# Kernel optimization log

Hardware: AMD Instinct MI355X
Metric: run time of the kernel (lower is better)

The kernel has to match this reference:

```python
import jax, jax.numpy as jnp
import numpy as np

Q = 3
MAX_SHIFT = 4.0


def setup_inputs() -> dict:
    key = jax.random.key(0)
    k1, k2, k3, k4 = jax.random.split(key, 4)
    x = jax.random.normal(k1, (16, 64, 128, 128), jnp.float32)
    weight = jax.random.normal(k2, (64, 192, 3, 3), jnp.float32) * 0.05
    bias = jax.random.normal(k3, (64,), jnp.float32) * 0.05
    # shift_init='random': uniform in [-1, 1]; forward multiplies by max_shift
    shifts = jax.random.uniform(k4, (64, 2), jnp.float32, -1.0, 1.0)
    return {"x": x, "weight": weight, "bias": bias, "shifts": shifts}


def _shift_bilinear(x, shifts, max_shift):
    """Per-channel bilinear translation, matching affine_grid+grid_sample
    (align_corners=False, padding_mode='zeros').
    x: [N,C,H,W]; shifts: [C,2] with (sx, sy) in normalized units.
    Sample location for output (i,j) is (i + sy*max_shift, j + sx*max_shift)."""
    N, C, H, W = x.shape
    sx = shifts[:, 0] * max_shift  # pixels along width
    sy = shifts[:, 1] * max_shift  # pixels along height
    ys = jnp.arange(H, dtype=x.dtype)[None, :] + sy[:, None]  # [C,H]
    xs = jnp.arange(W, dtype=x.dtype)[None, :] + sx[:, None]  # [C,W]
    y0f = jnp.floor(ys); fy = ys - y0f; y0 = y0f.astype(jnp.int32); y1 = y0 + 1
    x0f = jnp.floor(xs); fx = xs - x0f; x0 = x0f.astype(jnp.int32); x1 = x0 + 1

    def gather(yi, xi):
        vy = (yi >= 0) & (yi < H)          # [C,H]
        vx = (xi >= 0) & (xi < W)          # [C,W]
        yc = jnp.clip(yi, 0, H - 1)
        xc = jnp.clip(xi, 0, W - 1)
        g = jnp.take_along_axis(x, yc[None, :, :, None], axis=2)
        g = jnp.take_along_axis(g, xc[None, :, None, :], axis=3)
        m = (vy[:, :, None] & vx[:, None, :]).astype(x.dtype)[None]
        return g * m

    w00 = ((1 - fy)[:, :, None] * (1 - fx)[:, None, :])[None]
    w01 = ((1 - fy)[:, :, None] * fx[:, None, :])[None]
    w10 = (fy[:, :, None] * (1 - fx)[:, None, :])[None]
    w11 = (fy[:, :, None] * fx[:, None, :])[None]
    return (w00 * gather(y0, x0) + w01 * gather(y0, x1)
            + w10 * gather(y1, x0) + w11 * gather(y1, x1))


def reference(x, weight, bias, shifts):
    # 1) per-channel learnless shift (grid_sample bilinear, zeros padding)
    xs = _shift_bilinear(x, shifts, MAX_SHIFT)
    # 2) Maclaurin power series: concat(x, x^2, ..., x^q) on channels -> [N, C*q, H, W]
    xq = jnp.concatenate([xs ** i for i in range(1, Q + 1)], axis=1)
    # 3) dense conv (groups=1), stride 1, padding 1
    out = jax.lax.conv_general_dilated(
        xq, weight, window_strides=(1, 1), padding=((1, 1), (1, 1)),
        dimension_numbers=("NCHW", "OIHW", "NCHW"))
    return out + bias[None, :, None, None]
```

## Files before the change

kernel.cpp:

```cpp
#include <hip/hip_runtime.h>
#include <hip/hip_bf16.h>
#include <math.h>

#define NB 16
#define C_IN 64
#define C_OUT 64
#define HH 128
#define WW 128
#define MAX_SHIFT 4.0f

typedef __attribute__((ext_vector_type(8))) short bf16x8;
typedef __attribute__((ext_vector_type(4))) float f32x4;
typedef __attribute__((ext_vector_type(4))) unsigned int u32x4;

__device__ inline unsigned short bf16_rne(float f) {
    unsigned u = __builtin_bit_cast(unsigned, f);
    u += 0x7fffu + ((u >> 16) & 1u);
    return (unsigned short)(u >> 16);
}
__device__ inline unsigned pack_bf16x2(float lo, float hi) {
    unsigned ul = __builtin_bit_cast(unsigned, lo);
    unsigned uh = __builtin_bit_cast(unsigned, hi);
    ul += 0x7fffu + ((ul >> 16) & 1u);
    uh += 0x7fffu + ((uh >> 16) & 1u);
    return (ul >> 16) | (uh & 0xffff0000u);
}

#define VSTR 34

__global__ __launch_bounds__(256)
void shift_pow3(const float* __restrict__ x, const float* __restrict__ shifts,
                unsigned short* __restrict__ xsp) {
    __shared__ unsigned short row[128 * VSTR];
    __shared__ float s_fx[C_IN], s_fy[C_IN];
    __shared__ int s_dx[C_IN], s_dy[C_IN];

    int bid0 = blockIdx.x;
    int bid = (bid0 & 7) * 512 + (bid0 >> 3);
    int h  = bid & 127;
    int n  = (bid >> 7) & 15;
    int cg = bid >> 11;
    int tid = threadIdx.x;
    int wv = tid >> 6;
    int l  = tid & 63;

    if (tid < C_IN) {
        float sx = shifts[2 * tid] * MAX_SHIFT;
        float sy = shifts[2 * tid + 1] * MAX_SHIFT;
        float fx0 = floorf(sx), fy0 = floorf(sy);
        s_dx[tid] = (int)fx0; s_dy[tid] = (int)fy0;
        s_fx[tid] = sx - fx0;  s_fy[tid] = sy - fy0;
    }
    __syncthreads();

    const float* xn = x + (size_t)n * (C_IN * HH * WW);

    #pragma unroll 4
    for (int it = 0; it < 8; ++it) {
        int c32 = it * 4 + wv;
        int c   = cg * 32 + c32;
        int dx = s_dx[c], dy = s_dy[c];
        float fx = s_fx[c], fy = s_fy[c];
        const float* xp = xn + (size_t)c * (HH * WW);
        int y0 = h + dy, y1 = y0 + 1;
        bool vy0 = ((unsigned)y0 < (unsigned)HH);
        bool vy1 = ((unsigned)y1 < (unsigned)HH);
        const float* r0 = xp + y0 * WW;
        const float* r1 = xp + y1 * WW;

        #pragma unroll
        for (int hf = 0; hf < 2; ++hf) {
            int w = hf * 64 + l;
            int x0 = w + dx, x1 = x0 + 1;
            bool vx0 = ((unsigned)x0 < (unsigned)WW);
            bool vx1 = ((unsigned)x1 < (unsigned)WW);
            float v00 = (vy0 && vx0) ? r0[x0] : 0.f;
            float v01 = (vy0 && vx1) ? r0[x1] : 0.f;
            float v10 = (vy1 && vx0) ? r1[x0] : 0.f;
            float v11 = (vy1 && vx1) ? r1[x1] : 0.f;
            float v = (1.f - fy) * ((1.f - fx) * v00 + fx * v01)
                    + fy * ((1.f - fx) * v10 + fx * v11);
            row[w * VSTR + c32] = bf16_rne(v);
        }
    }
    __syncthreads();

    const unsigned* rp = (const unsigned*)row;
    unsigned* xsp32 = (unsigned*)xsp;
    #pragma unroll 1
    for (int p = 0; p < 3; ++p) {
        int kb = p * 2 + cg;
        unsigned* dst = xsp32 + (size_t)(kb * (NB * HH) + n * HH + h) * 2048;
        #pragma unroll
        for (int itw = 0; itw < 8; ++itw) {
            int o32 = itw * 256 + tid;
            int wl = o32 >> 4;
            int c4 = o32 & 15;
            unsigned u = rp[wl * 17 + c4];
            if (p != 0) {
                float f0 = __builtin_bit_cast(float, u << 16);
                float f1 = __builtin_bit_cast(float, u & 0xffff0000u);
                float r0 = f0 * f0, r1 = f1 * f1;
                if (p == 2) { r0 *= f0; r1 *= f1; }
                u = pack_bf16x2(r0, r1);
            }
            dst[o32] = u;
        }
    }
}

__global__ void prep_w2(const float* __restrict__ w, unsigned short* __restrict__ wbuf) {
    int id = blockIdx.x * 256 + threadIdx.x;
    int e = id & 7;
    int l = (id >> 3) & 63;
    int f = id >> 9;
    int mf = f & 3;
    int f2 = f >> 2;
    int kb = f2 % 6;
    int t  = f2 / 6;
    int k  = kb * 32 + (l >> 4) * 8 + e;
    int p  = k >> 6;
    int c  = k & 63;
    int co = mf * 16 + (l & 15);
    wbuf[id] = bf16_rne(w[(co * 192 + p * 64 + c) * 9 + t]);
}

__global__ __launch_bounds__(256, 2)
void conv2(const unsigned short* __restrict__ xsp,
           const unsigned short* __restrict__ wbuf,
           const float* __restrict__ bias,
           float* __restrict__ out) {
    __shared__ unsigned short tile[324 * 44];

    int bid = blockIdx.x;
    int wg = (bid & 7) * 128 + (bid >> 3);
    int n  = wg >> 6;
    int t6 = wg & 63;
    int i0 = (t6 >> 3) * 16;
    int j0 = (t6 & 7) * 16;

    int tid = threadIdx.x;
    int l  = tid & 63;
    int wv = tid >> 6;
    int lm = l & 15;
    int lg = l >> 4;

    f32x4 acc[4][4];
    #pragma unroll
    for (int mf = 0; mf < 4; ++mf) {
        #pragma unroll
        for (int r = 0; r < 4; ++r) {
            float bv = bias[mf * 16 + lg * 4 + r];
            #pragma unroll
            for (int nf = 0; nf < 4; ++nf) acc[mf][nf][r] = bv;
        }
    }

    int lds_base = (wv * 4 * 18 + lm) * 88 + lg * 16;

    #pragma unroll 1
    for (int kb = 0; kb < 6; ++kb) {
        const unsigned short* xr = xsp + (size_t)(kb * NB + n) * (HH * WW * 32);
        __syncthreads();
        #pragma unroll
        for (int it = 0; it < 6; ++it) {
            int ch = it * 256 + tid;
            if (ch < 1296) {
                int rr  = ch / 72;
                int rem = ch - rr * 72;
                int pxr = rem >> 2, sub = rem & 3;
                int gi = i0 - 1 + rr, gj = j0 - 1 + pxr;
                u32x4 d = {0, 0, 0, 0};
                if ((unsigned)gi < (unsigned)HH && (unsigned)gj < (unsigned)WW)
                    d = *(const u32x4*)(xr + ((size_t)gi * WW + gj) * 32 + sub * 8);
                *(u32x4*)((char*)tile + (rr * 18 + pxr) * 88 + sub * 16) = d;
            }
        }
        __syncthreads();

        __builtin_amdgcn_s_setprio(1);
        bf16x8 Af[4];
        #pragma unroll
        for (int mf = 0; mf < 4; ++mf)
            Af[mf] = *(const bf16x8*)(wbuf + (size_t)((0 * 6 + kb) * 4 + mf) * 512 + l * 8);

        #pragma unroll 1
        for (int t = 0; t < 9; ++t) {
            bf16x8 Afn[4];
            int tn = (t < 8) ? t + 1 : t;
            #pragma unroll
            for (int mf = 0; mf < 4; ++mf)
                Afn[mf] = *(const bf16x8*)(wbuf + (size_t)((tn * 6 + kb) * 4 + mf) * 512 + l * 8);

            int ky = t / 3, kx = t - ky * 3;
            #pragma unroll
            for (int nf = 0; nf < 4; ++nf) {
                int off = lds_base + ((nf + ky) * 18 + kx) * 88;
                bf16x8 bfrag = *(const bf16x8*)((const char*)tile + off);
                #pragma unroll
                for (int mf = 0; mf < 4; ++mf)
                    acc[mf][nf] = __builtin_amdgcn_mfma_f32_16x16x32_bf16(Af[mf], bfrag, acc[mf][nf], 0, 0, 0);
            }
            #pragma unroll
            for (int mf = 0; mf < 4; ++mf) Af[mf] = Afn[mf];
        }
        __builtin_amdgcn_s_setprio(0);
    }

    #pragma unroll
    for (int mf = 0; mf < 4; ++mf) {
        #pragma unroll
        for (int nf = 0; nf < 4; ++nf) {
            int rowi = i0 + wv * 4 + nf;
            int col = j0 + lm;
            #pragma unroll
            for (int r = 0; r < 4; ++r) {
                int co = mf * 16 + lg * 4 + r;
                out[(((size_t)n * C_OUT + co) * HH + rowi) * WW + col] = acc[mf][nf][r];
            }
        }
    }
}

#define S_PX 100

__global__ void prep_w3(const float* __restrict__ w, unsigned short* __restrict__ wbuf) {
    int id = blockIdx.x * 256 + threadIdx.x;
    int e = id & 7;
    int l = (id >> 3) & 63;
    int f = id >> 9;
    int mf = f & 3;
    int f2 = f >> 2;
    int kb = f2 % 6;
    int t  = f2 / 6;
    int cg = kb / 3;
    int p  = kb - cg * 3;
    int cl = (l >> 4) * 8 + e;
    int co = mf * 16 + (l & 15);
    wbuf[id] = bf16_rne(w[(co * 192 + p * 64 + cg * 32 + cl) * 9 + t]);
}

__global__ __launch_bounds__(256, 2)
void conv_f(const float* __restrict__ x,
            const float* __restrict__ shifts,
            const unsigned short* __restrict__ wbuf,
            const float* __restrict__ bias,
            float* __restrict__ out) {
    __shared__ unsigned short tile[324 * S_PX];
    __shared__ float s_fx[C_IN], s_fy[C_IN];
    __shared__ int s_dx[C_IN], s_dy[C_IN];

    int bid = blockIdx.x;
    int wg = (bid & 7) * 128 + (bid >> 3);
    int n  = wg >> 6;
    int t6 = wg & 63;
    int i0 = (t6 >> 3) * 16;
    int j0 = (t6 & 7) * 16;

    int tid = threadIdx.x;
    int l  = tid & 63;
    int wv = tid >> 6;
    int lm = l & 15;
    int lg = l >> 4;

    if (tid < C_IN) {
        float sx = shifts[2 * tid] * MAX_SHIFT;
        float sy = shifts[2 * tid + 1] * MAX_SHIFT;
        float fx0 = floorf(sx), fy0 = floorf(sy);
        s_dx[tid] = (int)fx0; s_dy[tid] = (int)fy0;
        s_fx[tid] = sx - fx0;  s_fy[tid] = sy - fy0;
    }

    f32x4 acc[4][4];
    #pragma unroll
    for (int mf = 0; mf < 4; ++mf) {
        #pragma unroll
        for (int r = 0; r < 4; ++r) {
            float bv = bias[mf * 16 + lg * 4 + r];
            #pragma unroll
            for (int nf = 0; nf < 4; ++nf) acc[mf][nf][r] = bv;
        }
    }

    const float* xn = x + (size_t)n * (C_IN * HH * WW);

    #pragma unroll 1
    for (int cg = 0; cg < 2; ++cg) {
        __syncthreads();
        #pragma unroll 2
        for (int it = 0; it < 21; ++it) {
            int item = it * 256 + tid;
            if (item < 5184) {
                int cl  = item / 162;
                int rem = item - cl * 162;
                int rp  = rem / 18;
                int cc  = rem - rp * 18;
                int c   = cg * 32 + cl;
                int dx = s_dx[c], dy = s_dy[c];
                float fx = s_fx[c], fy = s_fy[c];
                const float* xp = xn + (size_t)c * (HH * WW);

                int gj  = j0 - 1 + cc;
                int xx0 = gj + dx, xx1 = xx0 + 1;
                bool vx0 = ((unsigned)xx0 < (unsigned)WW);
                bool vx1 = ((unsigned)xx1 < (unsigned)WW);
                int gi0 = i0 - 1 + rp * 2;
                int y0  = gi0 + dy;
                bool vyA = ((unsigned)y0 < (unsigned)HH);
                bool vyB = ((unsigned)(y0 + 1) < (unsigned)HH);
                bool vyC = ((unsigned)(y0 + 2) < (unsigned)HH);
                const float* rA = xp + y0 * WW;
                const float* rB = rA + WW;
                const float* rC = rB + WW;
                float m0 = (vyA && vx0) ? rA[xx0] : 0.f;
                float m1 = (vyA && vx1) ? rA[xx1] : 0.f;
                float m2 = (vyB && vx0) ? rB[xx0] : 0.f;
                float m3 = (vyB && vx1) ? rB[xx1] : 0.f;
                float m4 = (vyC && vx0) ? rC[xx0] : 0.f;
                float m5 = (vyC && vx1) ? rC[xx1] : 0.f;
                float hA = (1.f - fx) * m0 + fx * m1;
                float hB = (1.f - fx) * m2 + fx * m3;
                float hC = (1.f - fx) * m4 + fx * m5;
                float vT = (1.f - fy) * hA + fy * hB;
                float vU = (1.f - fy) * hB + fy * hC;
                if (!((unsigned)gj < (unsigned)WW))        { vT = 0.f; vU = 0.f; }
                if (!((unsigned)gi0 < (unsigned)HH))       vT = 0.f;
                if (!((unsigned)(gi0 + 1) < (unsigned)HH)) vU = 0.f;

                float t2 = vT * vT, t3 = t2 * vT;
                float u2 = vU * vU, u3 = u2 * vU;
                unsigned short* recT = tile + (rp * 2 * 18 + cc) * S_PX;
                unsigned short* recU = recT + 18 * S_PX;
                recT[cl]      = bf16_rne(vT);
                recT[32 + cl] = bf16_rne(t2);
                recT[64 + cl] = bf16_rne(t3);
                recU[cl]      = bf16_rne(vU);
                recU[32 + cl] = bf16_rne(u2);
                recU[64 + cl] = bf16_rne(u3);
            }
        }
        __syncthreads();

        #pragma unroll 1
        for (int p = 0; p < 3; ++p) {
            int kb = cg * 3 + p;
            #pragma unroll 1
            for (int t = 0; t < 9; ++t) {
                bf16x8 Af[4];
                #pragma unroll
                for (int mf = 0; mf < 4; ++mf)
                    Af[mf] = *(const bf16x8*)(wbuf + (size_t)((t * 6 + kb) * 4 + mf) * 512 + l * 8);

                int ky = t / 3, kx = t - ky * 3;
                #pragma unroll
                for (int nf = 0; nf < 4; ++nf) {
                    int off = ((wv * 4 + nf + ky) * 18 + (lm + kx)) * 200 + p * 64 + lg * 16;
                    bf16x8 bfrag = *(const bf16x8*)((const char*)tile + off);
                    #pragma unroll
                    for (int mf = 0; mf < 4; ++mf)
                        acc[mf][nf] = __builtin_amdgcn_mfma_f32_16x16x32_bf16(Af[mf], bfrag, acc[mf][nf], 0, 0, 0);
                }
            }
        }
    }

    #pragma unroll
    for (int mf = 0; mf < 4; ++mf) {
        #pragma unroll
        for (int nf = 0; nf < 4; ++nf) {
            int rowi = i0 + wv * 4 + nf;
            int col = j0 + lm;
            #pragma unroll
            for (int r = 0; r < 4; ++r) {
                int co = mf * 16 + lg * 4 + r;
                out[(((size_t)n * C_OUT + co) * HH + rowi) * WW + col] = acc[mf][nf][r];
            }
        }
    }
}

extern "C" void kernel_launch(void* const* d_in, const int* in_sizes, int n_in,
                              void* d_out, int out_size, void* d_ws, size_t ws_size,
                              hipStream_t stream) {
    (void)in_sizes; (void)n_in; (void)out_size;
    const float* x      = (const float*)d_in[0];
    const float* weight = (const float*)d_in[1];
    const float* bias   = (const float*)d_in[2];
    const float* shifts = (const float*)d_in[3];
    float* out = (float*)d_out;

    const size_t xsp_elems = (size_t)6 * NB * HH * WW * 32;
    const size_t need2 = xsp_elems * 2 + 110592 * 2;

    if (ws_size >= need2) {
        unsigned short* xsp  = (unsigned short*)d_ws;
        unsigned short* wbuf = xsp + xsp_elems;
        prep_w2<<<432, 256, 0, stream>>>(weight, wbuf);
        shift_pow3<<<2 * NB * HH, 256, 0, stream>>>(x, shifts, xsp);
        conv2<<<1024, 256, 0, stream>>>(xsp, wbuf, bias, out);
    } else {
        unsigned short* wbuf = (unsigned short*)d_ws;
        prep_w3<<<432, 256, 0, stream>>>(weight, wbuf);
        conv_f<<<1024, 256, 0, stream>>>(x, shifts, wbuf, bias, out);
    }
}
```

Baseline: 93.54 us.

## Give each wave a private LDS halo tile to remove block barriers

```diff
diff --git a/kernel.cpp b/kernel.cpp
--- a/kernel.cpp
+++ b/kernel.cpp
@@ -125,12 +125,14 @@
     wbuf[id] = bf16_rne(w[(co * 192 + p * 64 + c) * 9 + t]);
 }
 
+#define WREG 11088
+
 __global__ __launch_bounds__(256, 2)
-void conv2(const unsigned short* __restrict__ xsp,
-           const unsigned short* __restrict__ wbuf,
-           const float* __restrict__ bias,
-           float* __restrict__ out) {
-    __shared__ unsigned short tile[324 * 44];
+void conv2h(const unsigned short* __restrict__ xsp,
+            const unsigned short* __restrict__ wbuf,
+            const float* __restrict__ bias,
+            float* __restrict__ out) {
+    __shared__ unsigned short tile[4 * WREG / 2];
 
     int bid = blockIdx.x;
     int wg = (bid & 7) * 128 + (bid >> 3);
@@ -156,29 +158,42 @@
         }
     }
 
-    int lds_base = (wv * 4 * 18 + lm) * 88 + lg * 16;
+    char* wbase = (char*)tile + wv * WREG;
+    int lds_rd = lm * 88 + lg * 16;
+
+    int soff[8];
+    int loff[8];
+    #pragma unroll
+    for (int it = 0; it < 8; ++it) {
+        int item = it * 64 + l;
+        soff[it] = -1;
+        loff[it] = 0;
+        if (item < 504) {
+            int px = item >> 2, sub = item & 3;
+            int q = px / 18, c = px - q * 18;
+            int gi = i0 - 1 + wv * 4 + q;
+            int gj = j0 - 1 + c;
+            loff[it] = px * 88 + sub * 16;
+            if ((unsigned)gi < (unsigned)HH && (unsigned)gj < (unsigned)WW)
+                soff[it] = (gi * WW + gj) * 32 + sub * 8;
+            else
+                soff[it] = -2;
+        }
+    }
 
     #pragma unroll 1
     for (int kb = 0; kb < 6; ++kb) {
         const unsigned short* xr = xsp + (size_t)(kb * NB + n) * (HH * WW * 32);
-        __syncthreads();
-        #pragma unroll
-        for (int it = 0; it < 6; ++it) {
-            int ch = it * 256 + tid;
-            if (ch < 1296) {
-                int rr  = ch / 72;
-                int rem = ch - rr * 72;
-                int pxr = rem >> 2, sub = rem & 3;
-                int gi = i0 - 1 + rr, gj = j0 - 1 + pxr;
+
+        #pragma unroll
+        for (int it = 0; it < 8; ++it) {
+            if (soff[it] != -1) {
                 u32x4 d = {0, 0, 0, 0};
-                if ((unsigned)gi < (unsigned)HH && (unsigned)gj < (unsigned)WW)
-                    d = *(const u32x4*)(xr + ((size_t)gi * WW + gj) * 32 + sub * 8);
-                *(u32x4*)((char*)tile + (rr * 18 + pxr) * 88 + sub * 16) = d;
-            }
-        }
-        __syncthreads();
-
-        __builtin_amdgcn_s_setprio(1);
+                if (soff[it] >= 0) d = *(const u32x4*)(xr + soff[it]);
+                *(u32x4*)(wbase + loff[it]) = d;
+            }
+        }
+
         bf16x8 Af[4];
         #pragma unroll
         for (int mf = 0; mf < 4; ++mf)
@@ -195,8 +210,8 @@
             int ky = t / 3, kx = t - ky * 3;
             #pragma unroll
             for (int nf = 0; nf < 4; ++nf) {
-                int off = lds_base + ((nf + ky) * 18 + kx) * 88;
-                bf16x8 bfrag = *(const bf16x8*)((const char*)tile + off);
+                int off = lds_rd + ((nf + ky) * 18 + kx) * 88;
+                bf16x8 bfrag = *(const bf16x8*)(wbase + off);
                 #pragma unroll
                 for (int mf = 0; mf < 4; ++mf)
                     acc[mf][nf] = __builtin_amdgcn_mfma_f32_16x16x32_bf16(Af[mf], bfrag, acc[mf][nf], 0, 0, 0);
@@ -204,7 +219,6 @@
             #pragma unroll
             for (int mf = 0; mf < 4; ++mf) Af[mf] = Afn[mf];
         }
-        __builtin_amdgcn_s_setprio(0);
     }
 
     #pragma unroll
@@ -397,7 +411,7 @@
         unsigned short* wbuf = xsp + xsp_elems;
         prep_w2<<<432, 256, 0, stream>>>(weight, wbuf);
         shift_pow3<<<2 * NB * HH, 256, 0, stream>>>(x, shifts, xsp);
-        conv2<<<1024, 256, 0, stream>>>(xsp, wbuf, bias, out);
+        conv2h<<<1024, 256, 0, stream>>>(xsp, wbuf, bias, out);
     } else {
         unsigned short* wbuf = (unsigned short*)d_ws;
         prep_w3<<<432, 256, 0, stream>>>(weight, wbuf);
```

After: 164.7 us. 1.76x slower.
